# Kernel tuning notes

Measured on AMD Instinct MI355X. Metric: run time of the kernel, lower is better.

Reference implementation:

```python
import jax, jax.numpy as jnp
import numpy as np

N = 50000        # num nodes
E = 800000       # num edges (before self loops)
F_DIM = 256      # embedding_dim
H = 4            # num_heads
C = 64           # latent_dim
SLOPE = 0.2      # PyG GATConv leaky_relu negative_slope


def setup_inputs() -> dict:
    key = jax.random.key(0)
    ks = jax.random.split(key, 11)
    s = 0.05
    return {
        "x": jax.random.normal(ks[0], (N, F_DIM), jnp.float32),
        "edge_index": jax.random.randint(ks[1], (2, E), 0, N),
        "W1": jax.random.normal(ks[2], (F_DIM, H * C), jnp.float32) * s,
        "a_src1": jax.random.normal(ks[3], (H, C), jnp.float32) * s,
        "a_dst1": jax.random.normal(ks[4], (H, C), jnp.float32) * s,
        "b1": jnp.zeros((H * C,), jnp.float32),
        "W2": jax.random.normal(ks[5], (H * C, F_DIM), jnp.float32) * s,
        "a_src2": jax.random.normal(ks[6], (1, F_DIM), jnp.float32) * s,
        "a_dst2": jax.random.normal(ks[7], (1, F_DIM), jnp.float32) * s,
        "b2": jnp.zeros((F_DIM,), jnp.float32),
    }


def gat_layer(x, src, dst, W, a_src, a_dst, bias, heads, out_ch):
    n = x.shape[0]
    xW = (x @ W).reshape(n, heads, out_ch)              # [N,H,C]
    alpha_s = jnp.sum(xW * a_src, axis=-1)               # [N,H]
    alpha_d = jnp.sum(xW * a_dst, axis=-1)               # [N,H]
    e = jax.nn.leaky_relu(alpha_s[src] + alpha_d[dst], SLOPE)  # [E,H]
    m = jax.ops.segment_max(e, dst, num_segments=n)      # segment-softmax over in-edges
    w = jnp.exp(e - m[dst])
    z = jax.ops.segment_sum(w, dst, num_segments=n)
    alpha = w / z[dst]                                    # [E,H]
    out = jax.ops.segment_sum(xW[src] * alpha[:, :, None], dst, num_segments=n)  # [N,H,C]
    return out.reshape(n, heads * out_ch) + bias          # concat=True


def reference(x, edge_index, W1, a_src1, a_dst1, b1, W2, a_src2, a_dst2, b2):
    loop = jnp.arange(N)  # PyG default add_self_loops=True
    src = jnp.concatenate([edge_index[0], loop])
    dst = jnp.concatenate([edge_index[1], loop])
    h = jax.nn.elu(gat_layer(x, src, dst, W1, a_src1, a_dst1, b1, H, C))
    return gat_layer(h, src, dst, W2, a_src2, a_dst2, b2, 1, F_DIM)
```

## Files before the change

### kernel.cpp

```cpp
#include <hip/hip_runtime.h>
#include <hip/hip_bf16.h>
#include <math.h>

#define N_NODES 50000
#define N_EDGES 800000
#define ETOT    (N_EDGES + N_NODES)
#define FDIM    256
#define SLOPE   0.2f

typedef __bf16    bf16x8 __attribute__((ext_vector_type(8)));
typedef float     f32x4  __attribute__((ext_vector_type(4)));
typedef _Float16  f16x8  __attribute__((ext_vector_type(8)));

__global__ void count_edges(const int* __restrict__ dst, int* __restrict__ counts) {
    int i = blockIdx.x * blockDim.x + threadIdx.x;
    if (i < N_EDGES) atomicAdd(&counts[dst[i]], 1);
}

__global__ void scan1(const int* __restrict__ counts, int* __restrict__ partial,
                      int* __restrict__ blockSums) {
    __shared__ int wsum[4];
    int b = blockIdx.x, t = threadIdx.x;
    int base = b * 1024;
    int i0 = base + t * 4;
    int v[4];
#pragma unroll
    for (int u = 0; u < 4; u++) { int i = i0 + u; v[u] = (i < N_NODES) ? (counts[i] + 1) : 0; }
    v[1] += v[0]; v[2] += v[1]; v[3] += v[2];
    int lane = t & 63, wid = t >> 6;
    int incl = v[3];
#pragma unroll
    for (int d = 1; d < 64; d <<= 1) {
        int o = __shfl_up(incl, d, 64);
        if (lane >= d) incl += o;
    }
    if (lane == 63) wsum[wid] = incl;
    __syncthreads();
    int woff = 0;
#pragma unroll
    for (int w = 0; w < 4; w++) if (w < wid) woff += wsum[w];
    int texcl = woff + incl - v[3];
#pragma unroll
    for (int u = 0; u < 4; u++) { int i = i0 + u; if (i < N_NODES) partial[i] = texcl + v[u]; }
    if (t == 255) blockSums[b] = woff + incl;
}

__global__ void scan2(int* __restrict__ blockSums, int nb) {
    int t = threadIdx.x;
    int v = (t < nb) ? blockSums[t] : 0;
    int incl = v;
#pragma unroll
    for (int d = 1; d < 64; d <<= 1) {
        int o = __shfl_up(incl, d, 64);
        if (t >= d) incl += o;
    }
    if (t < nb) blockSums[t] = incl - v;
}

__global__ void scan3(const int* __restrict__ partial, const int* __restrict__ blockOffs,
                      int* __restrict__ row_ptr, int* __restrict__ cursor) {
    int b = blockIdx.x, t = threadIdx.x;
    int base = b * 1024;
    int off = blockOffs[b];
#pragma unroll
    for (int u = 0; u < 4; u++) {
        int i = base + t + u * 256;
        if (i < N_NODES) {
            row_ptr[i + 1] = off + partial[i];
            cursor[i]      = off + ((i == base) ? 0 : partial[i - 1]);
        }
    }
    if (b == 0 && t == 0) row_ptr[0] = 0;
}

__global__ void scatter_edges(const int* __restrict__ src, const int* __restrict__ dst,
                              int* __restrict__ cursor, int* __restrict__ col_src) {
    int i = blockIdx.x * blockDim.x + threadIdx.x;
    if (i >= ETOT) return;
    int s, d;
    if (i < N_EDGES) { s = src[i]; d = dst[i]; }
    else             { s = i - N_EDGES; d = s; }
    int p = atomicAdd(&cursor[d], 1);
    col_src[p] = s;
}

__global__ void pack_w2(const float* __restrict__ W1, const float* __restrict__ W2,
                        __bf16* __restrict__ P1, __bf16* __restrict__ P2) {
    int tid = blockIdx.x * 256 + threadIdx.x;
    const float* W = (tid < 65536) ? W1 : W2;
    __bf16* P = (tid < 65536) ? P1 : P2;
    int t = tid & 65535;
    int j    = t & 7;
    int lane = (t >> 3) & 63;
    int nb   = (t >> 9) & 3;
    int w    = (t >> 11) & 3;
    int step = (t >> 13) & 7;
    int col = (w << 6) | (nb << 4) | (lane & 15);
    int k   = (step << 5) | ((lane >> 4) << 3) | j;
    float v = W[(k << 8) | col];
    __bf16 h = (__bf16)v;
    int base = (((((step << 2) | w) << 2) | nb) << 10) | (lane << 3) | j;
    P[base]       = h;
    P[base + 512] = (__bf16)(v - (float)h);
}

template <int HEADS>
__global__ __launch_bounds__(256) void gemm_mfma(
        const float* __restrict__ A, const __bf16* __restrict__ Bpk,
        _Float16* __restrict__ Ch,
        const float* __restrict__ avS, const float* __restrict__ avD,
        float* __restrict__ aS, float* __restrict__ aD, int M) {
    constexpr int LDA = 40;
    __shared__ __bf16 Ah[2][64 * LDA];
    __shared__ __bf16 Al[2][64 * LDA];
    __shared__ float sred[2][64][4];

    const int t = threadIdx.x;
    const int w = t >> 6, l = t & 63;
    const int q = l >> 4, c16 = l & 15;
    const int row0 = blockIdx.x * 64;

    const int ar = t >> 2, ak = (t & 3) << 3;
    const bool arow_ok = (row0 + ar) < M;
    const float* Arow = A + (size_t)(row0 + ar) * 256 + ak;

    f32x4 acc[4][4];
#pragma unroll
    for (int i = 0; i < 4; i++)
#pragma unroll
        for (int j = 0; j < 4; j++) acc[i][j] = (f32x4){0.f, 0.f, 0.f, 0.f};

    float4 pv0 = make_float4(0.f, 0.f, 0.f, 0.f), pv1 = pv0;
    if (arow_ok) {
        pv0 = *(const float4*)(Arow);
        pv1 = *(const float4*)(Arow + 4);
    }

    for (int step = 0; step < 8; ++step) {
        const int k0 = step << 5;
        const int buf = step & 1;

        {
            float vv[8] = {pv0.x, pv0.y, pv0.z, pv0.w, pv1.x, pv1.y, pv1.z, pv1.w};
            bf16x8 hv, lv;
#pragma unroll
            for (int j = 0; j < 8; j++) {
                __bf16 hb = (__bf16)vv[j];
                hv[j] = hb;
                lv[j] = (__bf16)(vv[j] - (float)hb);
            }
            *(bf16x8*)(&Ah[buf][ar * LDA + ak]) = hv;
            *(bf16x8*)(&Al[buf][ar * LDA + ak]) = lv;
        }
        if (step < 7 && arow_ok) {
            pv0 = *(const float4*)(Arow + k0 + 32);
            pv1 = *(const float4*)(Arow + k0 + 36);
        }
        const __bf16* Bs = Bpk + ((size_t)((step << 2) | w) << 12);
        bf16x8 bh[4], bl[4];
#pragma unroll
        for (int nb = 0; nb < 4; nb++) {
            bh[nb] = *(const bf16x8*)(Bs + (nb << 10) + (l << 3));
            bl[nb] = *(const bf16x8*)(Bs + (nb << 10) + 512 + (l << 3));
        }
        __syncthreads();

        bf16x8 ah[4], alo[4];
#pragma unroll
        for (int mb = 0; mb < 4; mb++) {
            int off = (c16 + (mb << 4)) * LDA + (q << 3);
            ah[mb]  = *(const bf16x8*)(&Ah[buf][off]);
            alo[mb] = *(const bf16x8*)(&Al[buf][off]);
        }
#pragma unroll
        for (int mb = 0; mb < 4; mb++)
#pragma unroll
            for (int nb = 0; nb < 4; nb++) {
                acc[mb][nb] = __builtin_amdgcn_mfma_f32_16x16x32_bf16(ah[mb],  bh[nb], acc[mb][nb], 0, 0, 0);
                acc[mb][nb] = __builtin_amdgcn_mfma_f32_16x16x32_bf16(ah[mb],  bl[nb], acc[mb][nb], 0, 0, 0);
                acc[mb][nb] = __builtin_amdgcn_mfma_f32_16x16x32_bf16(alo[mb], bh[nb], acc[mb][nb], 0, 0, 0);
            }
    }
    __syncthreads();

#pragma unroll
    for (int mb = 0; mb < 4; mb++) {
#pragma unroll
        for (int r = 0; r < 4; r++) {
            int row = (mb << 4) + (q << 2) + r;
            int grow = row0 + row;
            float s = 0.f, d = 0.f;
#pragma unroll
            for (int nb = 0; nb < 4; nb++) {
                int col = (w << 6) + (nb << 4) + c16;
                float val = acc[mb][nb][r];
                s = fmaf(val, avS[col], s);
                d = fmaf(val, avD[col], d);
                if (grow < M) Ch[(size_t)grow * 256 + col] = (_Float16)val;
            }
#pragma unroll
            for (int dd = 1; dd < 16; dd <<= 1) {
                s += __shfl_xor(s, dd, 64);
                d += __shfl_xor(d, dd, 64);
            }
            if (c16 == 0) { sred[0][row][w] = s; sred[1][row][w] = d; }
        }
    }
    __syncthreads();
    if (HEADS == 4) {
        int row = t >> 2, wv = t & 3;
        int v = row0 + row;
        if (v < M) { aS[v * 4 + wv] = sred[0][row][wv]; aD[v * 4 + wv] = sred[1][row][wv]; }
    } else {
        if (t < 64) {
            int v = row0 + t;
            if (v < M) {
                aS[v] = sred[0][t][0] + sred[0][t][1] + sred[0][t][2] + sred[0][t][3];
                aD[v] = sred[1][t][0] + sred[1][t][1] + sred[1][t][2] + sred[1][t][3];
            }
        }
    }
}

template <int HEADS, bool ELU>
__global__ __launch_bounds__(256) void gat_aggregate_wave(
        const _Float16* __restrict__ xWh, const float* __restrict__ aS,
        const float* __restrict__ aD, const int* __restrict__ row_ptr,
        const int* __restrict__ col_src, const float* __restrict__ bias,
        float* __restrict__ out) {
    const int wid  = threadIdx.x >> 6;
    const int lane = threadIdx.x & 63;
    const int v = blockIdx.x * 4 + wid;
    if (v >= N_NODES) return;

    constexpr int CH = 64 / HEADS;
    const int h = (HEADS == 4) ? (lane >> 4) : 0;
    const int q = (HEADS == 4) ? (lane & 15) : lane;

    const int half = lane >> 5;
    const int fl   = lane & 31;
    const int hf   = (HEADS == 4) ? (fl >> 3) : 0;
    const int wbase = (HEADS == 4) ? (hf << 4) : 0;

    const int beg = row_ptr[v], end = row_ptr[v + 1];
    const float adv = aD[v * HEADS + h];

    float acc[8] = {0.f, 0.f, 0.f, 0.f, 0.f, 0.f, 0.f, 0.f};
    float z = 0.f;
    for (int j0 = beg; j0 < end; j0 += CH) {
        const int cnt = min(CH, end - j0);
        int s = 0;
        float wgt = 0.f;
        if (q < cnt) {
            s = col_src[j0 + q];
            float e = aS[s * HEADS + h] + adv;
            e = (e > 0.f) ? e : SLOPE * e;
            wgt = __expf(e);
        }
        z += wgt;
        for (int jj = 0; jj < cnt; jj += 2) {
            const int qm = jj + half;
            const int sl = wbase | qm;
            const int   sj = __shfl(s,   sl, 64);
            const float wj = __shfl(wgt, sl, 64);
            if (qm < cnt) {
                const f16x8 row = *(const f16x8*)(xWh + ((size_t)sj << 8) + (fl << 3));
#pragma unroll
                for (int i = 0; i < 8; i++)
                    acc[i] = fmaf(wj, (float)row[i], acc[i]);
            }
        }
    }
#pragma unroll
    for (int d = 1; d < CH; d <<= 1) z += __shfl_xor(z, d, 64);
    const float zf = (HEADS == 4) ? __shfl(z, hf << 4, 64) : z;

#pragma unroll
    for (int i = 0; i < 8; i++) acc[i] += __shfl_xor(acc[i], 32, 64);

    const float rz = 1.f / zf;
    const int fbase = (fl << 3) + (half << 2);
    const float4 bv = *(const float4*)(bias + fbase);
    float4 o;
    o.x = acc[(half << 2) + 0] * rz + bv.x;
    o.y = acc[(half << 2) + 1] * rz + bv.y;
    o.z = acc[(half << 2) + 2] * rz + bv.z;
    o.w = acc[(half << 2) + 3] * rz + bv.w;
    if (ELU) {
        o.x = (o.x > 0.f) ? o.x : expm1f(o.x);
        o.y = (o.y > 0.f) ? o.y : expm1f(o.y);
        o.z = (o.z > 0.f) ? o.z : expm1f(o.z);
        o.w = (o.w > 0.f) ? o.w : expm1f(o.w);
    }
    *(float4*)(out + ((size_t)v << 8) + fbase) = o;
}

extern "C" void kernel_launch(void* const* d_in, const int* in_sizes, int n_in,
                              void* d_out, int out_size, void* d_ws, size_t ws_size,
                              hipStream_t stream) {
    const float* x   = (const float*)d_in[0];
    const int*   ei  = (const int*)d_in[1];
    const float* W1  = (const float*)d_in[2];
    const float* as1 = (const float*)d_in[3];
    const float* ad1 = (const float*)d_in[4];
    const float* b1  = (const float*)d_in[5];
    const float* W2  = (const float*)d_in[6];
    const float* as2 = (const float*)d_in[7];
    const float* ad2 = (const float*)d_in[8];
    const float* b2  = (const float*)d_in[9];
    float* out = (float*)d_out;

    const int* src = ei;
    const int* dst = ei + N_EDGES;

    char* w = (char*)d_ws;
    _Float16* xWh = (_Float16*)w; w += (size_t)N_NODES * 256 * 2;
    float* h  = (float*)w;  w += (size_t)N_NODES * 256 * 4;
    float* aS = (float*)w;  w += (size_t)N_NODES * 4 * 4;
    float* aD = (float*)w;  w += (size_t)N_NODES * 4 * 4;
    int* row_ptr = (int*)w; w += (((size_t)(N_NODES + 1) * 4 + 255) / 256) * 256;
    int* counts  = (int*)w; w += (((size_t)N_NODES * 4 + 255) / 256) * 256;
    int* cursor  = (int*)w; w += (((size_t)N_NODES * 4 + 255) / 256) * 256;
    int* partial = (int*)w; w += (((size_t)N_NODES * 4 + 255) / 256) * 256;
    int* bsums   = (int*)w; w += 256;
    int* col_src = (int*)w; w += (size_t)ETOT * 4;
    __bf16* Wpk1 = (__bf16*)w; w += 131072 * 2;
    __bf16* Wpk2 = (__bf16*)w; w += 131072 * 2;

    int nb = (N_NODES + 1023) / 1024;

    pack_w2<<<512, 256, 0, stream>>>(W1, W2, Wpk1, Wpk2);

    hipMemsetAsync(counts, 0, (size_t)N_NODES * 4, stream);
    count_edges<<<(N_EDGES + 255) / 256, 256, 0, stream>>>(dst, counts);
    scan1<<<nb, 256, 0, stream>>>(counts, partial, bsums);
    scan2<<<1, 64, 0, stream>>>(bsums, nb);
    scan3<<<nb, 256, 0, stream>>>(partial, bsums, row_ptr, cursor);
    scatter_edges<<<(ETOT + 255) / 256, 256, 0, stream>>>(src, dst, cursor, col_src);

    int gemm_blocks = (N_NODES + 63) / 64;
    int agg_blocks  = (N_NODES + 3) / 4;

    gemm_mfma<4><<<gemm_blocks, 256, 0, stream>>>(x, Wpk1, xWh, as1, ad1, aS, aD, N_NODES);
    gat_aggregate_wave<4, true><<<agg_blocks, 256, 0, stream>>>(xWh, aS, aD, row_ptr, col_src, b1, h);

    gemm_mfma<1><<<gemm_blocks, 256, 0, stream>>>(h, Wpk2, xWh, as2, ad2, aS, aD, N_NODES);
    gat_aggregate_wave<1, false><<<agg_blocks, 256, 0, stream>>>(xWh, aS, aD, row_ptr, col_src, b2, out);
}
```

Before: 313.2 us.

## Store hidden layer in fp16, stage GEMM output via LDS, fold scan2 into scan3

The intermediate hidden activation h is now written as fp16 by the first aggregation and read as fp16 by the second GEMM, halving that round-trip's traffic. The GEMM epilogue stages its fp16 output tile in shared memory, reusing the A-staging buffers through a union, then writes coalesced 16-byte rows instead of scattered 2-byte stores. The scan2 kernel is removed; each scan3 block reduces the preceding block sums itself, saving one launch. Rounding h to fp16 adds precision loss before the second layer.

```diff
diff --git a/kernel.cpp b/kernel.cpp
--- a/kernel.cpp
+++ b/kernel.cpp
@@ -11,6 +11,7 @@
 typedef __bf16    bf16x8 __attribute__((ext_vector_type(8)));
 typedef float     f32x4  __attribute__((ext_vector_type(4)));
 typedef _Float16  f16x8  __attribute__((ext_vector_type(8)));
+typedef _Float16  f16x4  __attribute__((ext_vector_type(4)));
 
 __global__ void count_edges(const int* __restrict__ dst, int* __restrict__ counts) {
     int i = blockIdx.x * blockDim.x + threadIdx.x;
@@ -45,23 +46,19 @@
     if (t == 255) blockSums[b] = woff + incl;
 }
 
-__global__ void scan2(int* __restrict__ blockSums, int nb) {
-    int t = threadIdx.x;
-    int v = (t < nb) ? blockSums[t] : 0;
-    int incl = v;
-#pragma unroll
-    for (int d = 1; d < 64; d <<= 1) {
-        int o = __shfl_up(incl, d, 64);
-        if (t >= d) incl += o;
-    }
-    if (t < nb) blockSums[t] = incl - v;
-}
-
-__global__ void scan3(const int* __restrict__ partial, const int* __restrict__ blockOffs,
+__global__ void scan3(const int* __restrict__ partial, const int* __restrict__ blockSums,
                       int* __restrict__ row_ptr, int* __restrict__ cursor) {
     int b = blockIdx.x, t = threadIdx.x;
+    __shared__ int s_off;
+    if (t < 64) {
+        int v = (t < b) ? blockSums[t] : 0;
+#pragma unroll
+        for (int d = 1; d < 64; d <<= 1) v += __shfl_xor(v, d, 64);
+        if (t == 0) s_off = v;
+    }
+    __syncthreads();
+    int off = s_off;
     int base = b * 1024;
-    int off = blockOffs[b];
 #pragma unroll
     for (int u = 0; u < 4; u++) {
         int i = base + t + u * 256;
@@ -104,15 +101,18 @@
     P[base + 512] = (__bf16)(v - (float)h);
 }
 
-template <int HEADS>
+template <int HEADS, typename AT>
 __global__ __launch_bounds__(256) void gemm_mfma(
-        const float* __restrict__ A, const __bf16* __restrict__ Bpk,
+        const AT* __restrict__ A, const __bf16* __restrict__ Bpk,
         _Float16* __restrict__ Ch,
         const float* __restrict__ avS, const float* __restrict__ avD,
         float* __restrict__ aS, float* __restrict__ aD, int M) {
     constexpr int LDA = 40;
-    __shared__ __bf16 Ah[2][64 * LDA];
-    __shared__ __bf16 Al[2][64 * LDA];
+    constexpr int LDC = 272;
+    __shared__ union SMem {
+        struct { __bf16 Ah[2][64 * LDA]; __bf16 Al[2][64 * LDA]; } st;
+        _Float16 cts[64][LDC];
+    } smem;
     __shared__ float sred[2][64][4];
 
     const int t = threadIdx.x;
@@ -122,7 +122,7 @@
 
     const int ar = t >> 2, ak = (t & 3) << 3;
     const bool arow_ok = (row0 + ar) < M;
-    const float* Arow = A + (size_t)(row0 + ar) * 256 + ak;
+    const AT* Arow = A + (size_t)(row0 + ar) * 256 + ak;
 
     f32x4 acc[4][4];
 #pragma unroll
@@ -131,9 +131,14 @@
         for (int j = 0; j < 4; j++) acc[i][j] = (f32x4){0.f, 0.f, 0.f, 0.f};
 
     float4 pv0 = make_float4(0.f, 0.f, 0.f, 0.f), pv1 = pv0;
+    f16x8  pvh = (f16x8){0, 0, 0, 0, 0, 0, 0, 0};
     if (arow_ok) {
-        pv0 = *(const float4*)(Arow);
-        pv1 = *(const float4*)(Arow + 4);
+        if constexpr (sizeof(AT) == 4) {
+            pv0 = *(const float4*)(Arow);
+            pv1 = *(const float4*)(Arow + 4);
+        } else {
+            pvh = *(const f16x8*)(Arow);
+        }
     }
 
     for (int step = 0; step < 8; ++step) {
@@ -141,7 +146,14 @@
         const int buf = step & 1;
 
         {
-            float vv[8] = {pv0.x, pv0.y, pv0.z, pv0.w, pv1.x, pv1.y, pv1.z, pv1.w};
+            float vv[8];
+            if constexpr (sizeof(AT) == 4) {
+                vv[0] = pv0.x; vv[1] = pv0.y; vv[2] = pv0.z; vv[3] = pv0.w;
+                vv[4] = pv1.x; vv[5] = pv1.y; vv[6] = pv1.z; vv[7] = pv1.w;
+            } else {
+#pragma unroll
+                for (int j = 0; j < 8; j++) vv[j] = (float)pvh[j];
+            }
             bf16x8 hv, lv;
 #pragma unroll
             for (int j = 0; j < 8; j++) {
@@ -149,12 +161,16 @@
                 hv[j] = hb;
                 lv[j] = (__bf16)(vv[j] - (float)hb);
             }
-            *(bf16x8*)(&Ah[buf][ar * LDA + ak]) = hv;
-            *(bf16x8*)(&Al[buf][ar * LDA + ak]) = lv;
+            *(bf16x8*)(&smem.st.Ah[buf][ar * LDA + ak]) = hv;
+            *(bf16x8*)(&smem.st.Al[buf][ar * LDA + ak]) = lv;
         }
         if (step < 7 && arow_ok) {
-            pv0 = *(const float4*)(Arow + k0 + 32);
-            pv1 = *(const float4*)(Arow + k0 + 36);
+            if constexpr (sizeof(AT) == 4) {
+                pv0 = *(const float4*)(Arow + k0 + 32);
+                pv1 = *(const float4*)(Arow + k0 + 36);
+            } else {
+                pvh = *(const f16x8*)(Arow + k0 + 32);
+            }
         }
         const __bf16* Bs = Bpk + ((size_t)((step << 2) | w) << 12);
         bf16x8 bh[4], bl[4];
@@ -169,8 +185,8 @@
 #pragma unroll
         for (int mb = 0; mb < 4; mb++) {
             int off = (c16 + (mb << 4)) * LDA + (q << 3);
-            ah[mb]  = *(const bf16x8*)(&Ah[buf][off]);
-            alo[mb] = *(const bf16x8*)(&Al[buf][off]);
+            ah[mb]  = *(const bf16x8*)(&smem.st.Ah[buf][off]);
+            alo[mb] = *(const bf16x8*)(&smem.st.Al[buf][off]);
         }
 #pragma unroll
         for (int mb = 0; mb < 4; mb++)
@@ -188,7 +204,6 @@
 #pragma unroll
         for (int r = 0; r < 4; r++) {
             int row = (mb << 4) + (q << 2) + r;
-            int grow = row0 + row;
             float s = 0.f, d = 0.f;
 #pragma unroll
             for (int nb = 0; nb < 4; nb++) {
@@ -196,7 +211,7 @@
                 float val = acc[mb][nb][r];
                 s = fmaf(val, avS[col], s);
                 d = fmaf(val, avD[col], d);
-                if (grow < M) Ch[(size_t)grow * 256 + col] = (_Float16)val;
+                smem.cts[row][col] = (_Float16)val;
             }
 #pragma unroll
             for (int dd = 1; dd < 16; dd <<= 1) {
@@ -207,6 +222,19 @@
         }
     }
     __syncthreads();
+
+    {
+        const int crow = t >> 2;
+        const int grow = row0 + crow;
+        if (grow < M) {
+            _Float16* dstp = Ch + (size_t)grow * 256;
+#pragma unroll
+            for (int i = 0; i < 8; i++) {
+                int col = ((t & 3) << 3) + (i << 5);
+                *(f16x8*)(dstp + col) = *(const f16x8*)(&smem.cts[crow][col]);
+            }
+        }
+    }
     if (HEADS == 4) {
         int row = t >> 2, wv = t & 3;
         int v = row0 + row;
@@ -222,12 +250,12 @@
     }
 }
 
-template <int HEADS, bool ELU>
+template <int HEADS, bool ELU, typename OT>
 __global__ __launch_bounds__(256) void gat_aggregate_wave(
         const _Float16* __restrict__ xWh, const float* __restrict__ aS,
         const float* __restrict__ aD, const int* __restrict__ row_ptr,
         const int* __restrict__ col_src, const float* __restrict__ bias,
-        float* __restrict__ out) {
+        OT* __restrict__ out) {
     const int wid  = threadIdx.x >> 6;
     const int lane = threadIdx.x & 63;
     const int v = blockIdx.x * 4 + wid;
@@ -292,7 +320,14 @@
         o.z = (o.z > 0.f) ? o.z : expm1f(o.z);
         o.w = (o.w > 0.f) ? o.w : expm1f(o.w);
     }
-    *(float4*)(out + ((size_t)v << 8) + fbase) = o;
+    if constexpr (sizeof(OT) == 2) {
+        f16x4 ov;
+        ov[0] = (_Float16)o.x; ov[1] = (_Float16)o.y;
+        ov[2] = (_Float16)o.z; ov[3] = (_Float16)o.w;
+        *(f16x4*)(out + ((size_t)v << 8) + fbase) = ov;
+    } else {
+        *(float4*)(out + ((size_t)v << 8) + fbase) = o;
+    }
 }
 
 extern "C" void kernel_launch(void* const* d_in, const int* in_sizes, int n_in,
@@ -315,7 +350,7 @@
 
     char* w = (char*)d_ws;
     _Float16* xWh = (_Float16*)w; w += (size_t)N_NODES * 256 * 2;
-    float* h  = (float*)w;  w += (size_t)N_NODES * 256 * 4;
+    _Float16* hh  = (_Float16*)w; w += (size_t)N_NODES * 256 * 2;
     float* aS = (float*)w;  w += (size_t)N_NODES * 4 * 4;
     float* aD = (float*)w;  w += (size_t)N_NODES * 4 * 4;
     int* row_ptr = (int*)w; w += (((size_t)(N_NODES + 1) * 4 + 255) / 256) * 256;
@@ -334,16 +369,15 @@
     hipMemsetAsync(counts, 0, (size_t)N_NODES * 4, stream);
     count_edges<<<(N_EDGES + 255) / 256, 256, 0, stream>>>(dst, counts);
     scan1<<<nb, 256, 0, stream>>>(counts, partial, bsums);
-    scan2<<<1, 64, 0, stream>>>(bsums, nb);
     scan3<<<nb, 256, 0, stream>>>(partial, bsums, row_ptr, cursor);
     scatter_edges<<<(ETOT + 255) / 256, 256, 0, stream>>>(src, dst, cursor, col_src);
 
     int gemm_blocks = (N_NODES + 63) / 64;
     int agg_blocks  = (N_NODES + 3) / 4;
 
-    gemm_mfma<4><<<gemm_blocks, 256, 0, stream>>>(x, Wpk1, xWh, as1, ad1, aS, aD, N_NODES);
-    gat_aggregate_wave<4, true><<<agg_blocks, 256, 0, stream>>>(xWh, aS, aD, row_ptr, col_src, b1, h);
-
-    gemm_mfma<1><<<gemm_blocks, 256, 0, stream>>>(h, Wpk2, xWh, as2, ad2, aS, aD, N_NODES);
-    gat_aggregate_wave<1, false><<<agg_blocks, 256, 0, stream>>>(xWh, aS, aD, row_ptr, col_src, b2, out);
-}
+    gemm_mfma<4, float><<<gemm_blocks, 256, 0, stream>>>(x, Wpk1, xWh, as1, ad1, aS, aD, N_NODES);
+    gat_aggregate_wave<4, true, _Float16><<<agg_blocks, 256, 0, stream>>>(xWh, aS, aD, row_ptr, col_src, b1, hh);
+
+    gemm_mfma<1, _Float16><<<gemm_blocks, 256, 0, stream>>>(hh, Wpk2, xWh, as2, ad2, aS, aD, N_NODES);
+    gat_aggregate_wave<1, false, float><<<agg_blocks, 256, 0, stream>>>(xWh, aS, aD, row_ptr, col_src, b2, out);
+}
```

Result: faster. 299.0 us (median of 2 runs) (-4.5%).
